# Kernel tuning notes

Measured on AMD Instinct MI355X. Metric: run time of the kernel, lower is better.

The kernel has to match this reference:

```python
import jax, jax.numpy as jnp
import numpy as np

N, D, W, S = 16384, 256, 64, 8  # utterances, embed dim, attention half-window, speakers


def setup_inputs() -> dict:
    key = jax.random.key(0)
    ks = jax.random.split(key, 8)
    scale = 1.0 / np.sqrt(D)
    return {
        "x": jax.random.normal(ks[0], (N, D), jnp.float32),
        "speaker_ids": jax.random.randint(ks[1], (N,), 0, S, jnp.int32),
        "W_att": jax.random.normal(ks[2], (D, D), jnp.float32) * scale,
        "W_pred": jax.random.normal(ks[3], (D, D), jnp.float32) * scale,
        "W_suc": jax.random.normal(ks[4], (D, D), jnp.float32) * scale,
        "W_same": jax.random.normal(ks[5], (D, D), jnp.float32) * scale,
        "W_diff": jax.random.normal(ks[6], (D, D), jnp.float32) * scale,
    }


def reference(x, speaker_ids, W_att, W_pred, W_suc, W_same, W_diff):
    n = x.shape[0]
    pad = jnp.zeros((W, D), x.dtype)
    # windowed gather: for utterance i, neighbors at offsets [-W, W-1] (2W slots)
    win_idx = jnp.arange(n)[:, None] + jnp.arange(2 * W)[None, :]  # index into padded [N+2W]
    xp = jnp.concatenate([pad, x, pad], axis=0)                    # [N+2W, D]
    windows = xp[win_idx]                                          # [N, 2W, D]
    # raw_attn[i,w] = (edge_att_weights(windows[i,w])) . x[i]
    raw_attn = jnp.einsum("nwd,ed,ne->nw", windows, W_att, x)      # [N, 2W]
    attn = jax.nn.softmax(raw_attn, axis=1)
    # relation masks over the band: j = i + offset
    offs = jnp.arange(2 * W) - W                                   # [-W, W-1]
    j = jnp.arange(n)[:, None] + offs[None, :]                     # [N, 2W]
    valid = (j >= 0) & (j < n)
    jc = jnp.clip(j, 0, n - 1)
    same_spk = speaker_ids[jc] == speaker_ids[:, None]
    masks = [
        valid & (offs >= 0)[None, :],   # pred: edges to current/future within window
        valid & (offs < 0)[None, :],    # suc: edges to past within window
        valid & same_spk,               # same speaker within window
        valid & ~same_spk,              # different speaker within window
    ]
    # relation-specific GCN aggregation: h = sum_r A_r @ (x @ W_r), A_r banded
    h = jnp.zeros_like(x)
    for Wr, m in zip([W_pred, W_suc, W_same, W_diff], masks):
        support = x @ Wr                                           # [N, D]
        sp = jnp.concatenate([pad, support, pad], axis=0)[win_idx]  # [N, 2W, D]
        h = h + jnp.einsum("nw,nwd->nd", attn * m, sp)
    return jax.nn.log_softmax(h, axis=1)
```

## Files before the change

### kernel.cpp

```cpp
#include <hip/hip_runtime.h>
#include <hip/hip_bf16.h>

typedef unsigned short u16;
typedef unsigned int u32;
typedef __attribute__((ext_vector_type(8))) short short8;
typedef __attribute__((ext_vector_type(4))) float floatx4;

#define NU 16384
#define DIM 256
#define AMS 208
#define ACS 200
#define ACM 12800

#define YLO 16896u
#define STGo 33792u
#define AMB 58368u

#define XHo 0u
#define XLo 4194304u
#define XRo 8388608u
#define ST0 20971520u
#define STROW 16512u
#define STMAT 4227072u
#define WH0o 33652736u
#define WL0o 33718272u
#define WRo  33783808u

__device__ __forceinline__ u16 bfh(float v) {
  return (u16)(__float_as_uint(v) >> 16);
}
__device__ __forceinline__ float bup(u16 u) {
  return __uint_as_float(((u32)u) << 16);
}
__device__ __forceinline__ u16 bfrn(float v) {
  u32 u = __float_as_uint(v);
  return (u16)((u + 0x7fffu + ((u >> 16) & 1u)) >> 16);
}

__device__ __forceinline__ void gload16(const u16* g, u16* l) {
  __builtin_amdgcn_global_load_lds(
      (__attribute__((address_space(1))) void*)(uintptr_t)g,
      (__attribute__((address_space(3))) void*)(uintptr_t)l, 16, 0, 0);
}

__global__ __launch_bounds__(256) void prep(
    const float* __restrict__ x,
    const float* __restrict__ wat, const float* __restrict__ wpr,
    const float* __restrict__ wsu, const float* __restrict__ wsm,
    const float* __restrict__ wdf, u16* __restrict__ ws) {
  const int b = blockIdx.x, t = threadIdx.x;
  if (b < 2048) {
    int idx = (b * 256 + t) * 8;
    float4 v0 = *(const float4*)(x + idx);
    float4 v1 = *(const float4*)(x + idx + 4);
    float a[8] = {v0.x, v0.y, v0.z, v0.w, v1.x, v1.y, v1.z, v1.w};
    u16 h[8], l[8], r[8];
#pragma unroll
    for (int q = 0; q < 8; ++q) {
      h[q] = bfh(a[q]);
      l[q] = bfh(a[q] - bup(h[q]));
      r[q] = bfrn(a[q]);
    }
    *(uint4*)(ws + XHo + idx) = *(const uint4*)h;
    *(uint4*)(ws + XLo + idx) = *(const uint4*)l;
    *(uint4*)(ws + XRo + idx) = *(const uint4*)r;
    return;
  }
  const int b2 = b - 2048;
  if (b2 < 32) {
    const int s = b2 & 7, mat = b2 >> 3, n = t;
    const float* Wa = (mat == 0) ? wat : (mat == 1) ? wpr : (mat == 2) ? wsm : wsu;
    const float* Wb = (mat == 0) ? wat : (mat == 1) ? wsu : (mat == 2) ? wdf : wdf;
    const float c1  = (mat == 0) ? 0.f : (mat == 3) ? 1.f : -1.f;
    u16 hbuf[32], lbuf[32];
#pragma unroll 8
    for (int k = 0; k < 32; ++k) {
      float v = Wa[(s * 32 + k) * 256 + n] + c1 * Wb[(s * 32 + k) * 256 + n];
      if (mat == 0) { hbuf[k] = bfh(v); lbuf[k] = bfh(v - bup(hbuf[k])); }
      else          { hbuf[k] = bfrn(v); }
    }
    u16* dh = ws + ((mat == 0) ? WH0o : (WRo + (size_t)(mat - 1) * 65536))
               + (size_t)s * 8192 + n * 32;
#pragma unroll
    for (int p = 0; p < 4; ++p) *(uint4*)(dh + p * 8) = ((const uint4*)hbuf)[p];
    if (mat == 0) {
      u16* dl = ws + WL0o + (size_t)s * 8192 + n * 32;
#pragma unroll
      for (int p = 0; p < 4; ++p) *(uint4*)(dl + p * 8) = ((const uint4*)lbuf)[p];
    }
  } else {
    int g = (b2 - 32) * 256 + t;
    int r = g >> 13, rem = g & 8191;
    int d = rem >> 5, p = rem & 31;
    size_t base = ST0 + (size_t)r * STMAT + (size_t)d * STROW;
    size_t off = (p < 16) ? (base + p * 4) : (base + 16448 + (p - 16) * 4);
    *(ushort4*)(ws + off) = make_ushort4(0, 0, 0, 0);
  }
}

__global__ __launch_bounds__(512, 4) void gemmS1(u16* __restrict__ ws) {
  __shared__ __align__(16) u16 U[39168];

  const int t = threadIdx.x, row0 = blockIdx.x * 32;
  const int w = t >> 6, ln = t & 15, quad = (t & 63) >> 4, q8 = quad * 8;
  const int n0 = w * 32;

#pragma unroll
  for (int cc = 0; cc < 2; ++cc) {
    int idx = t + 512 * cc;
    int row = idx >> 5, c8 = (idx & 31) * 8;
    *(uint4*)(U + row * 264 + c8) =
        *(const uint4*)(ws + XRo + (size_t)(row0 + row) * 256 + c8);
  }
  __syncthreads();

  floatx4 acc[3][2][2];
#pragma unroll
  for (int mat = 0; mat < 3; ++mat)
#pragma unroll
    for (int m = 0; m < 2; ++m)
#pragma unroll
      for (int nt = 0; nt < 2; ++nt) acc[mat][m][nt] = (floatx4){0.f, 0.f, 0.f, 0.f};

  for (int s = 0; s < 8; ++s) {
    short8 ah[2];
#pragma unroll
    for (int m = 0; m < 2; ++m)
      ah[m] = *(const short8*)(U + (m * 16 + ln) * 264 + s * 32 + q8);
#pragma unroll
    for (int mat = 0; mat < 3; ++mat) {
      short8 bh[2];
#pragma unroll
      for (int nt = 0; nt < 2; ++nt)
        bh[nt] = *(const short8*)(ws + WRo + (size_t)mat * 65536
                                  + (size_t)s * 8192 + (n0 + nt * 16 + ln) * 32 + q8);
#pragma unroll
      for (int m = 0; m < 2; ++m)
#pragma unroll
        for (int nt = 0; nt < 2; ++nt)
          acc[mat][m][nt] = __builtin_amdgcn_mfma_f32_16x16x32_bf16(ah[m], bh[nt], acc[mat][m][nt], 0, 0, 0);
    }
  }

#pragma unroll
  for (int mat = 0; mat < 3; ++mat)
#pragma unroll
    for (int m = 0; m < 2; ++m)
#pragma unroll
      for (int nt = 0; nt < 2; ++nt) {
        int col = n0 + nt * 16 + ln;
        ushort4 pk = make_ushort4(bfrn(acc[mat][m][nt][0]), bfrn(acc[mat][m][nt][1]),
                                  bfrn(acc[mat][m][nt][2]), bfrn(acc[mat][m][nt][3]));
        *(ushort4*)(U + 8448 + mat * 10240 + col * 40 + m * 16 + quad * 4) = pk;
      }
  __syncthreads();

#pragma unroll
  for (int mat = 0; mat < 3; ++mat)
#pragma unroll
    for (int cc = 0; cc < 2; ++cc) {
      int c = t + 512 * cc;
      int d = c >> 2, part = c & 3;
      *(uint4*)(ws + ST0 + (size_t)mat * STMAT + (size_t)d * STROW + 64 + row0 + part * 8) =
          *(const uint4*)(U + 8448 + mat * 10240 + d * 40 + part * 8);
    }
}

__global__ __launch_bounds__(512) void fused_attn(
    const u16* __restrict__ ws, const int* __restrict__ spk,
    float* __restrict__ out)
{
  __shared__ __align__(16) u16 U[71680];
  __shared__ int spkw[192];
  __shared__ float prt[64][2], prs[64][2];
  __shared__ float red[64][8];

  const int t    = threadIdx.x;
  const int w    = t >> 6;
  const int ln   = t & 15;
  const int quad = (t & 63) >> 4;
  const int q8   = quad * 8;
  const int bswz = (blockIdx.x & 7) * 32 + (blockIdx.x >> 3);
  const int i0   = bswz * 64;
  const int mw   = w & 3;
  const int half = w >> 2;
  const int n0   = w * 32;

  if (t < 192) spkw[t] = spk[min(max(i0 - 64 + t, 0), NU - 1)];

  {
#pragma unroll
    for (int cc = 0; cc < 8; ++cc) {
      int idx = t + 512 * cc;
      int buf = idx >> 11, e = idx & 2047;
      int row = e >> 5, c8 = (e & 31) * 8;
      *(uint4*)(U + buf * YLO + row * 264 + c8) =
          *(const uint4*)(ws + (buf ? XLo : XHo) + (size_t)(i0 + row) * 256 + c8);
    }
    __syncthreads();

    floatx4 acc[4][2];
#pragma unroll
    for (int m = 0; m < 4; ++m)
#pragma unroll
      for (int nt = 0; nt < 2; ++nt) acc[m][nt] = (floatx4){0.f, 0.f, 0.f, 0.f};

    for (int s = 0; s < 8; ++s) {
      short8 ah[4], al[4];
#pragma unroll
      for (int m = 0; m < 4; ++m) {
        ah[m] = *(const short8*)(U + (m * 16 + ln) * 264 + s * 32 + q8);
        al[m] = *(const short8*)(U + YLO + (m * 16 + ln) * 264 + s * 32 + q8);
      }
      short8 bh[2], bl[2];
#pragma unroll
      for (int nt = 0; nt < 2; ++nt) {
        size_t off = (size_t)s * 8192 + (n0 + nt * 16 + ln) * 32 + q8;
        bh[nt] = *(const short8*)(ws + WH0o + off);
        bl[nt] = *(const short8*)(ws + WL0o + off);
      }
#pragma unroll
      for (int m = 0; m < 4; ++m)
#pragma unroll
        for (int nt = 0; nt < 2; ++nt) {
          acc[m][nt] = __builtin_amdgcn_mfma_f32_16x16x32_bf16(ah[m], bh[nt], acc[m][nt], 0, 0, 0);
          acc[m][nt] = __builtin_amdgcn_mfma_f32_16x16x32_bf16(ah[m], bl[nt], acc[m][nt], 0, 0, 0);
          acc[m][nt] = __builtin_amdgcn_mfma_f32_16x16x32_bf16(al[m], bh[nt], acc[m][nt], 0, 0, 0);
        }
    }
    __syncthreads();

#pragma unroll
    for (int m = 0; m < 4; ++m)
#pragma unroll
      for (int nt = 0; nt < 2; ++nt) {
        int col = n0 + nt * 16 + ln;
#pragma unroll
        for (int r = 0; r < 4; ++r) {
          int row = m * 16 + quad * 4 + r;
          float y = acc[m][nt][r];
          u16 hh = bfh(y);
          U[row * 264 + col] = hh;
          U[YLO + row * 264 + col] = bfh(y - bup(hh));
        }
      }
  }

  auto STAGE = [&](int ks, int par) {
    const int kd = ks * 32;
    u16* db = U + STGo + par * 12288;
#pragma unroll
    for (int cc = 0; cc < 3; ++cc) {
      int idx  = t + 512 * cc;
      int bsel = (idx >= 768) ? 1 : 0;
      int e    = idx - bsel * 768;
      int row  = e >> 2, s = e & 3;
      int sw   = s ^ ((row >> 1) & 3);
      int jc   = min(max(i0 + row - 64, 0), NU - 1);
      const u16* src = ws + (bsel ? XLo : XHo) + (size_t)jc * 256 + kd + sw * 8;
      u16* dst = db + bsel * 6144 + e * 8;
      gload16(src, dst);
    }
  };

  floatx4 accP[6];
#pragma unroll
  for (int cc = 0; cc < 6; ++cc) accP[cc] = (floatx4){0.f, 0.f, 0.f, 0.f};

  STAGE(0, 0);
  __syncthreads();
#pragma unroll
  for (int ks = 0; ks < 8; ++ks) {
    if (ks < 7) STAGE(ks + 1, (ks + 1) & 1);
    const u16* sp = U + STGo + (ks & 1) * 12288;
    const u16* yb = U + (mw * 16 + ln) * 264 + ks * 32 + q8;
    short8 yh8 = *(const short8*)yb;
    short8 yl8 = *(const short8*)(yb + YLO);
#pragma unroll
    for (int cc = 0; cc < 6; ++cc) {
      int xrow = half * 96 + cc * 16 + ln;
      int slot = quad ^ ((xrow >> 1) & 3);
      const u16* xb = sp + xrow * 32 + slot * 8;
      short8 xbh = *(const short8*)xb;
      short8 xbl = *(const short8*)(xb + 6144);
      accP[cc] = __builtin_amdgcn_mfma_f32_16x16x32_bf16(yh8, xbh, accP[cc], 0, 0, 0);
      accP[cc] = __builtin_amdgcn_mfma_f32_16x16x32_bf16(yh8, xbl, accP[cc], 0, 0, 0);
      accP[cc] = __builtin_amdgcn_mfma_f32_16x16x32_bf16(yl8, xbh, accP[cc], 0, 0, 0);
    }
    __syncthreads();
  }

  int  c_of[6];
  bool vj[6];
#pragma unroll
  for (int cc = 0; cc < 6; ++cc) {
    c_of[cc] = half * 96 + cc * 16 + ln;
    int j = i0 + c_of[cc] - 64;
    vj[cc] = (j >= 0) && (j < NU);
  }
#pragma unroll
  for (int r = 0; r < 4; ++r) {
    int row = mw * 16 + quad * 4 + r;
    float mx = -3.4e38f;
#pragma unroll
    for (int cc = 0; cc < 6; ++cc) {
      int rel = c_of[cc] - row;
      bool inb = (rel >= 0) && (rel < 128);
      if (inb) mx = fmaxf(mx, vj[cc] ? accP[cc][r] : 0.f);
    }
#pragma unroll
    for (int o = 1; o < 16; o <<= 1) mx = fmaxf(mx, __shfl_xor(mx, o));
    if (ln == 0) prt[row][half] = mx;
  }
  __syncthreads();
#pragma unroll
  for (int r = 0; r < 4; ++r) {
    int row = mw * 16 + quad * 4 + r;
    float gm = fmaxf(prt[row][0], prt[row][1]);
    float s = 0.f;
#pragma unroll
    for (int cc = 0; cc < 6; ++cc) {
      int rel = c_of[cc] - row;
      bool inb = (rel >= 0) && (rel < 128);
      float vv = vj[cc] ? accP[cc][r] : 0.f;
      float e  = inb ? __expf(vv - gm) : 0.f;
      s += e;
      accP[cc][r] = (inb && vj[cc]) ? e : 0.f;
    }
#pragma unroll
    for (int o = 1; o < 16; o <<= 1) s += __shfl_xor(s, o);
    if (ln == 0) prs[row][half] = s;
  }
  __syncthreads();
#pragma unroll
  for (int r = 0; r < 4; ++r) {
    int row = mw * 16 + quad * 4 + r;
    float inv = 1.f / (prs[row][0] + prs[row][1]);
#pragma unroll
    for (int cc = 0; cc < 6; ++cc)
      U[AMB + row * AMS + c_of[cc]] = bfrn(accP[cc][r] * inv);
  }
  __syncthreads();

  {
    const int arow = t >> 3, aseg = t & 7;
    const int sr = spkw[arow + 64];
#pragma unroll
    for (int c6 = 0; c6 < 6; ++c6) {
      int cb = c6 * 32 + aseg * 4;
      ushort4 av = *(const ushort4*)(U + AMB + arow * AMS + cb);
      u16 aq[4] = {av.x, av.y, av.z, av.w};
      u16 b0[4], b1[4], b2[4];
#pragma unroll
      for (int q = 0; q < 4; ++q) {
        int c = cb + q;
        b0[q] = (c - arow >= 64) ? aq[q] : (u16)0;
        b1[q] = (spkw[c] == sr) ? aq[q] : (u16)0;
        b2[q] = aq[q];
      }
      *(ushort4*)(U + 0 * ACM + arow * ACS + cb) = *(const ushort4*)b0;
      *(ushort4*)(U + 1 * ACM + arow * ACS + cb) = *(const ushort4*)b1;
      *(ushort4*)(U + 2 * ACM + arow * ACS + cb) = *(const ushort4*)b2;
    }
  }
  __syncthreads();

  floatx4 acc2[4][2];
#pragma unroll
  for (int m = 0; m < 4; ++m)
#pragma unroll
    for (int nt = 0; nt < 2; ++nt) acc2[m][nt] = (floatx4){0.f, 0.f, 0.f, 0.f};

  for (int kj = 0; kj < 192; kj += 32) {
#pragma unroll
    for (int rel = 0; rel < 3; ++rel) {
      short8 af[4];
#pragma unroll
      for (int m = 0; m < 4; ++m)
        af[m] = *(const short8*)(U + rel * ACM + (m * 16 + ln) * ACS + kj + q8);
#pragma unroll
      for (int nt = 0; nt < 2; ++nt) {
        size_t so = (size_t)ST0 + (size_t)rel * STMAT
                  + (size_t)(n0 + nt * 16 + ln) * STROW + (size_t)(i0 + kj) + q8;
        short8 bf8 = *(const short8*)(ws + so);
#pragma unroll
        for (int m = 0; m < 4; ++m)
          acc2[m][nt] = __builtin_amdgcn_mfma_f32_16x16x32_bf16(af[m], bf8, acc2[m][nt], 0, 0, 0);
      }
    }
  }

#pragma unroll
  for (int m = 0; m < 4; ++m)
#pragma unroll
    for (int r = 0; r < 4; ++r) {
      float v = fmaxf(acc2[m][0][r], acc2[m][1][r]);
#pragma unroll
      for (int o = 1; o < 16; o <<= 1) v = fmaxf(v, __shfl_xor(v, o));
      if (ln == 0) red[m * 16 + quad * 4 + r][w] = v;
    }
  __syncthreads();
  float gmx[4][4];
#pragma unroll
  for (int m = 0; m < 4; ++m)
#pragma unroll
    for (int r = 0; r < 4; ++r) {
      int row = m * 16 + quad * 4 + r;
      float g = red[row][0];
#pragma unroll
      for (int ww = 1; ww < 8; ++ww) g = fmaxf(g, red[row][ww]);
      gmx[m][r] = g;
    }
  __syncthreads();
#pragma unroll
  for (int m = 0; m < 4; ++m)
#pragma unroll
    for (int r = 0; r < 4; ++r) {
      float e = __expf(acc2[m][0][r] - gmx[m][r]) + __expf(acc2[m][1][r] - gmx[m][r]);
#pragma unroll
      for (int o = 1; o < 16; o <<= 1) e += __shfl_xor(e, o);
      if (ln == 0) red[m * 16 + quad * 4 + r][w] = e;
    }
  __syncthreads();
#pragma unroll
  for (int m = 0; m < 4; ++m)
#pragma unroll
    for (int r = 0; r < 4; ++r) {
      int row = m * 16 + quad * 4 + r;
      float s = red[row][0];
#pragma unroll
      for (int ww = 1; ww < 8; ++ww) s += red[row][ww];
      float lse = gmx[m][r] + logf(s);
      size_t rowg = (size_t)(i0 + row) * DIM;
      out[rowg + n0 + ln]      = acc2[m][0][r] - lse;
      out[rowg + n0 + 16 + ln] = acc2[m][1][r] - lse;
    }
}

extern "C" void kernel_launch(void* const* d_in, const int* in_sizes, int n_in,
                              void* d_out, int out_size, void* d_ws, size_t ws_size,
                              hipStream_t stream) {
  const float* x   = (const float*)d_in[0];
  const int*   spk = (const int*)d_in[1];
  const float* wat = (const float*)d_in[2];
  const float* wpr = (const float*)d_in[3];
  const float* wsu = (const float*)d_in[4];
  const float* wsm = (const float*)d_in[5];
  const float* wdf = (const float*)d_in[6];
  float* out = (float*)d_out;
  u16* ws = (u16*)d_ws;

  hipLaunchKernelGGL(prep, dim3(2176), dim3(256), 0, stream,
                     x, wat, wpr, wsu, wsm, wdf, ws);
  hipLaunchKernelGGL(gemmS1, dim3(512), dim3(512), 0, stream, ws);
  hipLaunchKernelGGL(fused_attn, dim3(256), dim3(512), 0, stream, ws, spk, out);
}
```

Before: 146.9 us.

## Widen fused_attn to 1024 threads, drop LDS staging, skip masked relation tiles

Doubles the fused_attn block to 1024 threads so each wave owns 16 output columns. The block-level LDS double-buffered staging of neighbor rows is removed; waves load x hi/lo fragments straight from global memory. The relation-0 (causal) mask matrix is no longer materialised. It is applied in registers, and K-tiles that are fully masked are skipped, which cuts LDS footprint and redundant MFMAs. The intent is more waves per block, fewer barriers and less shared memory. The trade-off is more uncoalesced global reads and wider 16-way cross-wave reductions.

New measurement: 185.7 us. +26.3%, slower.

```diff
diff --git a/kernel.cpp b/kernel.cpp
--- a/kernel.cpp
+++ b/kernel.cpp
@@ -8,13 +8,9 @@
 
 #define NU 16384
 #define DIM 256
-#define AMS 208
-#define ACS 200
-#define ACM 12800
-
+#define AMS 200
+#define AC1 12800u
 #define YLO 16896u
-#define STGo 33792u
-#define AMB 58368u
 
 #define XHo 0u
 #define XLo 4194304u
@@ -35,12 +31,6 @@
 __device__ __forceinline__ u16 bfrn(float v) {
   u32 u = __float_as_uint(v);
   return (u16)((u + 0x7fffu + ((u >> 16) & 1u)) >> 16);
-}
-
-__device__ __forceinline__ void gload16(const u16* g, u16* l) {
-  __builtin_amdgcn_global_load_lds(
-      (__attribute__((address_space(1))) void*)(uintptr_t)g,
-      (__attribute__((address_space(3))) void*)(uintptr_t)l, 16, 0, 0);
 }
 
 __global__ __launch_bounds__(256) void prep(
@@ -166,14 +156,14 @@
     }
 }
 
-__global__ __launch_bounds__(512) void fused_attn(
+__global__ __launch_bounds__(1024, 4) void fused_attn(
     const u16* __restrict__ ws, const int* __restrict__ spk,
     float* __restrict__ out)
 {
-  __shared__ __align__(16) u16 U[71680];
+  __shared__ __align__(16) u16 U[33792];
   __shared__ int spkw[192];
-  __shared__ float prt[64][2], prs[64][2];
-  __shared__ float red[64][8];
+  __shared__ float prt[64][4], prs[64][4];
+  __shared__ float red[64][16];
 
   const int t    = threadIdx.x;
   const int w    = t >> 6;
@@ -183,15 +173,15 @@
   const int bswz = (blockIdx.x & 7) * 32 + (blockIdx.x >> 3);
   const int i0   = bswz * 64;
   const int mw   = w & 3;
-  const int half = w >> 2;
-  const int n0   = w * 32;
+  const int halfq = w >> 2;
+  const int n0   = w * 16;
 
   if (t < 192) spkw[t] = spk[min(max(i0 - 64 + t, 0), NU - 1)];
 
   {
 #pragma unroll
-    for (int cc = 0; cc < 8; ++cc) {
-      int idx = t + 512 * cc;
+    for (int cc = 0; cc < 4; ++cc) {
+      int idx = t + 1024 * cc;
       int buf = idx >> 11, e = idx & 2047;
       int row = e >> 5, c8 = (e & 31) * 8;
       *(uint4*)(U + buf * YLO + row * 264 + c8) =
@@ -199,11 +189,9 @@
     }
     __syncthreads();
 
-    floatx4 acc[4][2];
-#pragma unroll
-    for (int m = 0; m < 4; ++m)
-#pragma unroll
-      for (int nt = 0; nt < 2; ++nt) acc[m][nt] = (floatx4){0.f, 0.f, 0.f, 0.f};
+    floatx4 acc[4];
+#pragma unroll
+    for (int m = 0; m < 4; ++m) acc[m] = (floatx4){0.f, 0.f, 0.f, 0.f};
 
     for (int s = 0; s < 8; ++s) {
       short8 ah[4], al[4];
@@ -212,89 +200,60 @@
         ah[m] = *(const short8*)(U + (m * 16 + ln) * 264 + s * 32 + q8);
         al[m] = *(const short8*)(U + YLO + (m * 16 + ln) * 264 + s * 32 + q8);
       }
-      short8 bh[2], bl[2];
-#pragma unroll
-      for (int nt = 0; nt < 2; ++nt) {
-        size_t off = (size_t)s * 8192 + (n0 + nt * 16 + ln) * 32 + q8;
-        bh[nt] = *(const short8*)(ws + WH0o + off);
-        bl[nt] = *(const short8*)(ws + WL0o + off);
-      }
-#pragma unroll
-      for (int m = 0; m < 4; ++m)
-#pragma unroll
-        for (int nt = 0; nt < 2; ++nt) {
-          acc[m][nt] = __builtin_amdgcn_mfma_f32_16x16x32_bf16(ah[m], bh[nt], acc[m][nt], 0, 0, 0);
-          acc[m][nt] = __builtin_amdgcn_mfma_f32_16x16x32_bf16(ah[m], bl[nt], acc[m][nt], 0, 0, 0);
-          acc[m][nt] = __builtin_amdgcn_mfma_f32_16x16x32_bf16(al[m], bh[nt], acc[m][nt], 0, 0, 0);
-        }
+      size_t off = (size_t)s * 8192 + (n0 + ln) * 32 + q8;
+      short8 bh = *(const short8*)(ws + WH0o + off);
+      short8 bl = *(const short8*)(ws + WL0o + off);
+#pragma unroll
+      for (int m = 0; m < 4; ++m) {
+        acc[m] = __builtin_amdgcn_mfma_f32_16x16x32_bf16(ah[m], bh, acc[m], 0, 0, 0);
+        acc[m] = __builtin_amdgcn_mfma_f32_16x16x32_bf16(ah[m], bl, acc[m], 0, 0, 0);
+        acc[m] = __builtin_amdgcn_mfma_f32_16x16x32_bf16(al[m], bh, acc[m], 0, 0, 0);
+      }
     }
     __syncthreads();
 
 #pragma unroll
-    for (int m = 0; m < 4; ++m)
-#pragma unroll
-      for (int nt = 0; nt < 2; ++nt) {
-        int col = n0 + nt * 16 + ln;
-#pragma unroll
-        for (int r = 0; r < 4; ++r) {
-          int row = m * 16 + quad * 4 + r;
-          float y = acc[m][nt][r];
-          u16 hh = bfh(y);
-          U[row * 264 + col] = hh;
-          U[YLO + row * 264 + col] = bfh(y - bup(hh));
-        }
-      }
-  }
-
-  auto STAGE = [&](int ks, int par) {
-    const int kd = ks * 32;
-    u16* db = U + STGo + par * 12288;
-#pragma unroll
-    for (int cc = 0; cc < 3; ++cc) {
-      int idx  = t + 512 * cc;
-      int bsel = (idx >= 768) ? 1 : 0;
-      int e    = idx - bsel * 768;
-      int row  = e >> 2, s = e & 3;
-      int sw   = s ^ ((row >> 1) & 3);
-      int jc   = min(max(i0 + row - 64, 0), NU - 1);
-      const u16* src = ws + (bsel ? XLo : XHo) + (size_t)jc * 256 + kd + sw * 8;
-      u16* dst = db + bsel * 6144 + e * 8;
-      gload16(src, dst);
-    }
-  };
-
-  floatx4 accP[6];
-#pragma unroll
-  for (int cc = 0; cc < 6; ++cc) accP[cc] = (floatx4){0.f, 0.f, 0.f, 0.f};
-
-  STAGE(0, 0);
-  __syncthreads();
-#pragma unroll
+    for (int m = 0; m < 4; ++m) {
+      int col = n0 + ln;
+#pragma unroll
+      for (int r = 0; r < 4; ++r) {
+        int row = m * 16 + quad * 4 + r;
+        float y = acc[m][r];
+        u16 hh = bfh(y);
+        U[row * 264 + col] = hh;
+        U[YLO + row * 264 + col] = bfh(y - bup(hh));
+      }
+    }
+  }
+  __syncthreads();
+
+  floatx4 accP[3];
+#pragma unroll
+  for (int cc = 0; cc < 3; ++cc) accP[cc] = (floatx4){0.f, 0.f, 0.f, 0.f};
+
+#pragma unroll 2
   for (int ks = 0; ks < 8; ++ks) {
-    if (ks < 7) STAGE(ks + 1, (ks + 1) & 1);
-    const u16* sp = U + STGo + (ks & 1) * 12288;
     const u16* yb = U + (mw * 16 + ln) * 264 + ks * 32 + q8;
     short8 yh8 = *(const short8*)yb;
     short8 yl8 = *(const short8*)(yb + YLO);
 #pragma unroll
-    for (int cc = 0; cc < 6; ++cc) {
-      int xrow = half * 96 + cc * 16 + ln;
-      int slot = quad ^ ((xrow >> 1) & 3);
-      const u16* xb = sp + xrow * 32 + slot * 8;
-      short8 xbh = *(const short8*)xb;
-      short8 xbl = *(const short8*)(xb + 6144);
+    for (int cc = 0; cc < 3; ++cc) {
+      int xrow = halfq * 48 + cc * 16 + ln;
+      int jc = min(max(i0 + xrow - 64, 0), NU - 1);
+      size_t xo = (size_t)jc * 256 + ks * 32 + q8;
+      short8 xbh = *(const short8*)(ws + XHo + xo);
+      short8 xbl = *(const short8*)(ws + XLo + xo);
       accP[cc] = __builtin_amdgcn_mfma_f32_16x16x32_bf16(yh8, xbh, accP[cc], 0, 0, 0);
       accP[cc] = __builtin_amdgcn_mfma_f32_16x16x32_bf16(yh8, xbl, accP[cc], 0, 0, 0);
       accP[cc] = __builtin_amdgcn_mfma_f32_16x16x32_bf16(yl8, xbh, accP[cc], 0, 0, 0);
     }
-    __syncthreads();
-  }
-
-  int  c_of[6];
-  bool vj[6];
-#pragma unroll
-  for (int cc = 0; cc < 6; ++cc) {
-    c_of[cc] = half * 96 + cc * 16 + ln;
+  }
+
+  int  c_of[3];
+  bool vj[3];
+#pragma unroll
+  for (int cc = 0; cc < 3; ++cc) {
+    c_of[cc] = halfq * 48 + cc * 16 + ln;
     int j = i0 + c_of[cc] - 64;
     vj[cc] = (j >= 0) && (j < NU);
   }
@@ -303,23 +262,23 @@
     int row = mw * 16 + quad * 4 + r;
     float mx = -3.4e38f;
 #pragma unroll
-    for (int cc = 0; cc < 6; ++cc) {
+    for (int cc = 0; cc < 3; ++cc) {
       int rel = c_of[cc] - row;
       bool inb = (rel >= 0) && (rel < 128);
       if (inb) mx = fmaxf(mx, vj[cc] ? accP[cc][r] : 0.f);
     }
 #pragma unroll
     for (int o = 1; o < 16; o <<= 1) mx = fmaxf(mx, __shfl_xor(mx, o));
-    if (ln == 0) prt[row][half] = mx;
+    if (ln == 0) prt[row][halfq] = mx;
   }
   __syncthreads();
 #pragma unroll
   for (int r = 0; r < 4; ++r) {
     int row = mw * 16 + quad * 4 + r;
-    float gm = fmaxf(prt[row][0], prt[row][1]);
+    float gm = fmaxf(fmaxf(prt[row][0], prt[row][1]), fmaxf(prt[row][2], prt[row][3]));
     float s = 0.f;
 #pragma unroll
-    for (int cc = 0; cc < 6; ++cc) {
+    for (int cc = 0; cc < 3; ++cc) {
       int rel = c_of[cc] - row;
       bool inb = (rel >= 0) && (rel < 128);
       float vv = vj[cc] ? accP[cc][r] : 0.f;
@@ -329,72 +288,81 @@
     }
 #pragma unroll
     for (int o = 1; o < 16; o <<= 1) s += __shfl_xor(s, o);
-    if (ln == 0) prs[row][half] = s;
+    if (ln == 0) prs[row][halfq] = s;
   }
   __syncthreads();
 #pragma unroll
   for (int r = 0; r < 4; ++r) {
     int row = mw * 16 + quad * 4 + r;
-    float inv = 1.f / (prs[row][0] + prs[row][1]);
-#pragma unroll
-    for (int cc = 0; cc < 6; ++cc)
-      U[AMB + row * AMS + c_of[cc]] = bfrn(accP[cc][r] * inv);
+    float inv = 1.f / (prs[row][0] + prs[row][1] + prs[row][2] + prs[row][3]);
+#pragma unroll
+    for (int cc = 0; cc < 3; ++cc)
+      U[row * AMS + c_of[cc]] = bfrn(accP[cc][r] * inv);
   }
   __syncthreads();
 
   {
-    const int arow = t >> 3, aseg = t & 7;
+    const int arow = t >> 4, aseg = t & 15;
     const int sr = spkw[arow + 64];
-#pragma unroll
-    for (int c6 = 0; c6 < 6; ++c6) {
-      int cb = c6 * 32 + aseg * 4;
-      ushort4 av = *(const ushort4*)(U + AMB + arow * AMS + cb);
+    const int cb = aseg * 12;
+#pragma unroll
+    for (int p = 0; p < 3; ++p) {
+      ushort4 av = *(const ushort4*)(U + arow * AMS + cb + p * 4);
       u16 aq[4] = {av.x, av.y, av.z, av.w};
-      u16 b0[4], b1[4], b2[4];
+      u16 b1v[4];
 #pragma unroll
       for (int q = 0; q < 4; ++q) {
-        int c = cb + q;
-        b0[q] = (c - arow >= 64) ? aq[q] : (u16)0;
-        b1[q] = (spkw[c] == sr) ? aq[q] : (u16)0;
-        b2[q] = aq[q];
-      }
-      *(ushort4*)(U + 0 * ACM + arow * ACS + cb) = *(const ushort4*)b0;
-      *(ushort4*)(U + 1 * ACM + arow * ACS + cb) = *(const ushort4*)b1;
-      *(ushort4*)(U + 2 * ACM + arow * ACS + cb) = *(const ushort4*)b2;
-    }
-  }
-  __syncthreads();
-
-  floatx4 acc2[4][2];
+        int c = cb + p * 4 + q;
+        b1v[q] = (spkw[c] == sr) ? aq[q] : (u16)0;
+      }
+      *(ushort4*)(U + AC1 + arow * AMS + cb + p * 4) = *(const ushort4*)b1v;
+    }
+  }
+  __syncthreads();
+
+  floatx4 acc2[4];
+#pragma unroll
+  for (int m = 0; m < 4; ++m) acc2[m] = (floatx4){0.f, 0.f, 0.f, 0.f};
+
+#pragma unroll
+  for (int kj = 0; kj < 6; ++kj) {
+    short8 af[4], af1[4];
+#pragma unroll
+    for (int m = 0; m < 4; ++m) {
+      af[m]  = *(const short8*)(U + (m * 16 + ln) * AMS + kj * 32 + q8);
+      af1[m] = *(const short8*)(U + AC1 + (m * 16 + ln) * AMS + kj * 32 + q8);
+    }
+    size_t sbase = (size_t)ST0 + (size_t)(n0 + ln) * STROW + (size_t)(i0 + kj * 32) + q8;
+    short8 b2 = *(const short8*)(ws + sbase + 2 * (size_t)STMAT);
+    short8 b1 = *(const short8*)(ws + sbase + 1 * (size_t)STMAT);
+#pragma unroll
+    for (int m = 0; m < 4; ++m)
+      acc2[m] = __builtin_amdgcn_mfma_f32_16x16x32_bf16(af[m], b2, acc2[m], 0, 0, 0);
+#pragma unroll
+    for (int m = 0; m < 4; ++m)
+      acc2[m] = __builtin_amdgcn_mfma_f32_16x16x32_bf16(af1[m], b1, acc2[m], 0, 0, 0);
+    if (kj >= 2) {
+      short8 b0 = *(const short8*)(ws + sbase);
+#pragma unroll
+      for (int m = 0; m < 4; ++m) {
+        if (32 * kj < 16 * m + 33) continue;
+        short8 a0 = af[m];
+        if (!(32 * kj >= 16 * m + 79)) {
+          int tthr = m * 16 + ln + 64 - kj * 32 - q8;
+#pragma unroll
+          for (int e = 0; e < 8; ++e)
+            if (e < tthr) a0[e] = 0;
+        }
+        acc2[m] = __builtin_amdgcn_mfma_f32_16x16x32_bf16(a0, b0, acc2[m], 0, 0, 0);
+      }
+    }
+  }
+
 #pragma unroll
   for (int m = 0; m < 4; ++m)
 #pragma unroll
-    for (int nt = 0; nt < 2; ++nt) acc2[m][nt] = (floatx4){0.f, 0.f, 0.f, 0.f};
-
-  for (int kj = 0; kj < 192; kj += 32) {
-#pragma unroll
-    for (int rel = 0; rel < 3; ++rel) {
-      short8 af[4];
-#pragma unroll
-      for (int m = 0; m < 4; ++m)
-        af[m] = *(const short8*)(U + rel * ACM + (m * 16 + ln) * ACS + kj + q8);
-#pragma unroll
-      for (int nt = 0; nt < 2; ++nt) {
-        size_t so = (size_t)ST0 + (size_t)rel * STMAT
-                  + (size_t)(n0 + nt * 16 + ln) * STROW + (size_t)(i0 + kj) + q8;
-        short8 bf8 = *(const short8*)(ws + so);
-#pragma unroll
-        for (int m = 0; m < 4; ++m)
-          acc2[m][nt] = __builtin_amdgcn_mfma_f32_16x16x32_bf16(af[m], bf8, acc2[m][nt], 0, 0, 0);
-      }
-    }
-  }
-
-#pragma unroll
-  for (int m = 0; m < 4; ++m)
-#pragma unroll
     for (int r = 0; r < 4; ++r) {
-      float v = fmaxf(acc2[m][0][r], acc2[m][1][r]);
+      float v = acc2[m][r];
 #pragma unroll
       for (int o = 1; o < 16; o <<= 1) v = fmaxf(v, __shfl_xor(v, o));
       if (ln == 0) red[m * 16 + quad * 4 + r][w] = v;
@@ -408,7 +376,7 @@
       int row = m * 16 + quad * 4 + r;
       float g = red[row][0];
 #pragma unroll
-      for (int ww = 1; ww < 8; ++ww) g = fmaxf(g, red[row][ww]);
+      for (int ww = 1; ww < 16; ++ww) g = fmaxf(g, red[row][ww]);
       gmx[m][r] = g;
     }
   __syncthreads();
@@ -416,7 +384,7 @@
   for (int m = 0; m < 4; ++m)
 #pragma unroll
     for (int r = 0; r < 4; ++r) {
-      float e = __expf(acc2[m][0][r] - gmx[m][r]) + __expf(acc2[m][1][r] - gmx[m][r]);
+      float e = __expf(acc2[m][r] - gmx[m][r]);
 #pragma unroll
       for (int o = 1; o < 16; o <<= 1) e += __shfl_xor(e, o);
       if (ln == 0) red[m * 16 + quad * 4 + r][w] = e;
@@ -429,11 +397,10 @@
       int row = m * 16 + quad * 4 + r;
       float s = red[row][0];
 #pragma unroll
-      for (int ww = 1; ww < 8; ++ww) s += red[row][ww];
+      for (int ww = 1; ww < 16; ++ww) s += red[row][ww];
       float lse = gmx[m][r] + logf(s);
       size_t rowg = (size_t)(i0 + row) * DIM;
-      out[rowg + n0 + ln]      = acc2[m][0][r] - lse;
-      out[rowg + n0 + 16 + ln] = acc2[m][1][r] - lse;
+      out[rowg + n0 + ln] = acc2[m][r] - lse;
     }
 }
 
@@ -453,5 +420,5 @@
   hipLaunchKernelGGL(prep, dim3(2176), dim3(256), 0, stream,
                      x, wat, wpr, wsu, wsm, wdf, ws);
   hipLaunchKernelGGL(gemmS1, dim3(512), dim3(512), 0, stream, ws);
-  hipLaunchKernelGGL(fused_attn, dim3(256), dim3(512), 0, stream, ws, spk, out);
-}
+  hipLaunchKernelGGL(fused_attn, dim3(256), dim3(1024), 0, stream, ws, spk, out);
+}
```

## Drop LDS staging of X tiles and compute pred mask in registers to cut LDS

Applied to the files above, without the earlier changes.

Removes the double-buffered global-to-LDS staging of the x hi/lo windows. The score GEMM now reads x fragments directly from global memory through per-lane pointers, with no per-step barriers. The pred-masked attention matrix is no longer stored; the mask is applied to register fragments, and MFMAs on fully masked blocks are skipped. Together this shrinks LDS from about 143KB to about 68KB and adds a launch-bounds occupancy hint, trading redundant global/L2 reads for more resident blocks and fewer barriers.

Measured after the change: 166.4 us. 1.13x slower.

```diff
diff --git a/kernel.cpp b/kernel.cpp
--- a/kernel.cpp
+++ b/kernel.cpp
@@ -8,13 +8,9 @@
 
 #define NU 16384
 #define DIM 256
-#define AMS 208
-#define ACS 200
-#define ACM 12800
-
+#define AMS 200
+#define AC1o 12800u
 #define YLO 16896u
-#define STGo 33792u
-#define AMB 58368u
 
 #define XHo 0u
 #define XLo 4194304u
@@ -35,12 +31,6 @@
 __device__ __forceinline__ u16 bfrn(float v) {
   u32 u = __float_as_uint(v);
   return (u16)((u + 0x7fffu + ((u >> 16) & 1u)) >> 16);
-}
-
-__device__ __forceinline__ void gload16(const u16* g, u16* l) {
-  __builtin_amdgcn_global_load_lds(
-      (__attribute__((address_space(1))) void*)(uintptr_t)g,
-      (__attribute__((address_space(3))) void*)(uintptr_t)l, 16, 0, 0);
 }
 
 __global__ __launch_bounds__(256) void prep(
@@ -166,11 +156,11 @@
     }
 }
 
-__global__ __launch_bounds__(512) void fused_attn(
+__global__ __launch_bounds__(512, 4) void fused_attn(
     const u16* __restrict__ ws, const int* __restrict__ spk,
     float* __restrict__ out)
 {
-  __shared__ __align__(16) u16 U[71680];
+  __shared__ __align__(16) u16 U[33792];
   __shared__ int spkw[192];
   __shared__ float prt[64][2], prs[64][2];
   __shared__ float red[64][8];
@@ -245,49 +235,35 @@
         }
       }
   }
-
-  auto STAGE = [&](int ks, int par) {
-    const int kd = ks * 32;
-    u16* db = U + STGo + par * 12288;
-#pragma unroll
-    for (int cc = 0; cc < 3; ++cc) {
-      int idx  = t + 512 * cc;
-      int bsel = (idx >= 768) ? 1 : 0;
-      int e    = idx - bsel * 768;
-      int row  = e >> 2, s = e & 3;
-      int sw   = s ^ ((row >> 1) & 3);
-      int jc   = min(max(i0 + row - 64, 0), NU - 1);
-      const u16* src = ws + (bsel ? XLo : XHo) + (size_t)jc * 256 + kd + sw * 8;
-      u16* dst = db + bsel * 6144 + e * 8;
-      gload16(src, dst);
-    }
-  };
+  __syncthreads();
 
   floatx4 accP[6];
 #pragma unroll
   for (int cc = 0; cc < 6; ++cc) accP[cc] = (floatx4){0.f, 0.f, 0.f, 0.f};
 
-  STAGE(0, 0);
-  __syncthreads();
-#pragma unroll
+  const u16* xb_h[6];
+  const u16* xb_l[6];
+#pragma unroll
+  for (int cc = 0; cc < 6; ++cc) {
+    int xrow = half * 96 + cc * 16 + ln;
+    int jc = min(max(i0 + xrow - 64, 0), NU - 1);
+    xb_h[cc] = ws + XHo + (size_t)jc * 256 + q8;
+    xb_l[cc] = ws + XLo + (size_t)jc * 256 + q8;
+  }
+
+#pragma unroll 2
   for (int ks = 0; ks < 8; ++ks) {
-    if (ks < 7) STAGE(ks + 1, (ks + 1) & 1);
-    const u16* sp = U + STGo + (ks & 1) * 12288;
     const u16* yb = U + (mw * 16 + ln) * 264 + ks * 32 + q8;
     short8 yh8 = *(const short8*)yb;
     short8 yl8 = *(const short8*)(yb + YLO);
 #pragma unroll
     for (int cc = 0; cc < 6; ++cc) {
-      int xrow = half * 96 + cc * 16 + ln;
-      int slot = quad ^ ((xrow >> 1) & 3);
-      const u16* xb = sp + xrow * 32 + slot * 8;
-      short8 xbh = *(const short8*)xb;
-      short8 xbl = *(const short8*)(xb + 6144);
+      short8 xbh = *(const short8*)(xb_h[cc] + ks * 32);
+      short8 xbl = *(const short8*)(xb_l[cc] + ks * 32);
       accP[cc] = __builtin_amdgcn_mfma_f32_16x16x32_bf16(yh8, xbh, accP[cc], 0, 0, 0);
       accP[cc] = __builtin_amdgcn_mfma_f32_16x16x32_bf16(yh8, xbl, accP[cc], 0, 0, 0);
       accP[cc] = __builtin_amdgcn_mfma_f32_16x16x32_bf16(yl8, xbh, accP[cc], 0, 0, 0);
     }
-    __syncthreads();
   }
 
   int  c_of[6];
@@ -338,29 +314,25 @@
     float inv = 1.f / (prs[row][0] + prs[row][1]);
 #pragma unroll
     for (int cc = 0; cc < 6; ++cc)
-      U[AMB + row * AMS + c_of[cc]] = bfrn(accP[cc][r] * inv);
+      U[row * AMS + c_of[cc]] = bfrn(accP[cc][r] * inv);
   }
   __syncthreads();
 
   {
     const int arow = t >> 3, aseg = t & 7;
     const int sr = spkw[arow + 64];
-#pragma unroll
-    for (int c6 = 0; c6 < 6; ++c6) {
-      int cb = c6 * 32 + aseg * 4;
-      ushort4 av = *(const ushort4*)(U + AMB + arow * AMS + cb);
+    const int cb = aseg * 24;
+#pragma unroll
+    for (int p = 0; p < 6; ++p) {
+      ushort4 av = *(const ushort4*)(U + arow * AMS + cb + p * 4);
       u16 aq[4] = {av.x, av.y, av.z, av.w};
-      u16 b0[4], b1[4], b2[4];
+      u16 b1v[4];
 #pragma unroll
       for (int q = 0; q < 4; ++q) {
-        int c = cb + q;
-        b0[q] = (c - arow >= 64) ? aq[q] : (u16)0;
-        b1[q] = (spkw[c] == sr) ? aq[q] : (u16)0;
-        b2[q] = aq[q];
-      }
-      *(ushort4*)(U + 0 * ACM + arow * ACS + cb) = *(const ushort4*)b0;
-      *(ushort4*)(U + 1 * ACM + arow * ACS + cb) = *(const ushort4*)b1;
-      *(ushort4*)(U + 2 * ACM + arow * ACS + cb) = *(const ushort4*)b2;
+        int c = cb + p * 4 + q;
+        b1v[q] = (spkw[c] == sr) ? aq[q] : (u16)0;
+      }
+      *(ushort4*)(U + AC1o + arow * AMS + cb + p * 4) = *(const ushort4*)b1v;
     }
   }
   __syncthreads();
@@ -371,21 +343,49 @@
 #pragma unroll
     for (int nt = 0; nt < 2; ++nt) acc2[m][nt] = (floatx4){0.f, 0.f, 0.f, 0.f};
 
-  for (int kj = 0; kj < 192; kj += 32) {
-#pragma unroll
-    for (int rel = 0; rel < 3; ++rel) {
-      short8 af[4];
-#pragma unroll
-      for (int m = 0; m < 4; ++m)
-        af[m] = *(const short8*)(U + rel * ACM + (m * 16 + ln) * ACS + kj + q8);
+#pragma unroll
+  for (int kj = 0; kj < 6; ++kj) {
+    short8 af[4], af1[4];
+#pragma unroll
+    for (int m = 0; m < 4; ++m) {
+      af[m]  = *(const short8*)(U + (m * 16 + ln) * AMS + kj * 32 + q8);
+      af1[m] = *(const short8*)(U + AC1o + (m * 16 + ln) * AMS + kj * 32 + q8);
+    }
+    size_t sb[2];
+#pragma unroll
+    for (int nt = 0; nt < 2; ++nt)
+      sb[nt] = (size_t)ST0 + (size_t)(n0 + nt * 16 + ln) * STROW
+             + (size_t)(i0 + kj * 32) + q8;
+#pragma unroll
+    for (int nt = 0; nt < 2; ++nt) {
+      short8 b2 = *(const short8*)(ws + sb[nt] + 2 * (size_t)STMAT);
+      short8 b1 = *(const short8*)(ws + sb[nt] + 1 * (size_t)STMAT);
+#pragma unroll
+      for (int m = 0; m < 4; ++m) {
+        acc2[m][nt] = __builtin_amdgcn_mfma_f32_16x16x32_bf16(af[m],  b2, acc2[m][nt], 0, 0, 0);
+        acc2[m][nt] = __builtin_amdgcn_mfma_f32_16x16x32_bf16(af1[m], b1, acc2[m][nt], 0, 0, 0);
+      }
+    }
+    if (kj >= 2) {
+      short8 a0m[4];
+#pragma unroll
+      for (int m = 0; m < 4; ++m) {
+        a0m[m] = af[m];
+        if (!(32 * kj >= 16 * m + 79)) {
+          int tthr = m * 16 + ln + 64 - kj * 32 - q8;
+#pragma unroll
+          for (int e = 0; e < 8; ++e)
+            if (e < tthr) a0m[m][e] = 0;
+        }
+      }
 #pragma unroll
       for (int nt = 0; nt < 2; ++nt) {
-        size_t so = (size_t)ST0 + (size_t)rel * STMAT
-                  + (size_t)(n0 + nt * 16 + ln) * STROW + (size_t)(i0 + kj) + q8;
-        short8 bf8 = *(const short8*)(ws + so);
-#pragma unroll
-        for (int m = 0; m < 4; ++m)
-          acc2[m][nt] = __builtin_amdgcn_mfma_f32_16x16x32_bf16(af[m], bf8, acc2[m][nt], 0, 0, 0);
+        short8 b0 = *(const short8*)(ws + sb[nt]);
+#pragma unroll
+        for (int m = 0; m < 4; ++m) {
+          if (32 * kj < 16 * m + 33) continue;
+          acc2[m][nt] = __builtin_amdgcn_mfma_f32_16x16x32_bf16(a0m[m], b0, acc2[m][nt], 0, 0, 0);
+        }
       }
     }
   }
```
